# Optimization experiments

Measured on AMD Instinct MI355X. Metric: run time of the kernel, lower is better.

Reference implementation:

```python
import jax, jax.numpy as jnp
import numpy as np
import math

N_HEADS = 8
INPUT_DIM = 128
EMBED_DIM = 128
KEY_DIM = EMBED_DIM // N_HEADS  # 16, val_dim == key_dim
BATCH = 4
GRAPH = 2048


def setup_inputs() -> dict:
    key = jax.random.key(0)
    k1, k2, k3, k4, k5 = jax.random.split(key, 5)
    h = jax.random.normal(k1, (BATCH, GRAPH, INPUT_DIM), dtype=jnp.float32)
    # torch.rand -> uniform [0,1)
    W_query = jax.random.uniform(k2, (N_HEADS, INPUT_DIM, KEY_DIM), dtype=jnp.float32)
    W_key = jax.random.uniform(k3, (N_HEADS, INPUT_DIM, KEY_DIM), dtype=jnp.float32)
    W_val = jax.random.uniform(k4, (N_HEADS, INPUT_DIM, KEY_DIM), dtype=jnp.float32)
    W_out = jax.random.uniform(k5, (N_HEADS, KEY_DIM, EMBED_DIM), dtype=jnp.float32)
    return {"h": h, "W_query": W_query, "W_key": W_key, "W_val": W_val, "W_out": W_out}


def reference(h, W_query, W_key, W_val, W_out):
    # q defaults to h (self-attention)
    norm = 1.0 / math.sqrt(KEY_DIM)
    # per-head projections: [H, B, N, dk]
    Q = jnp.einsum('bnd,hdk->hbnk', h, W_query)
    K = jnp.einsum('bnd,hdk->hbnk', h, W_key)
    V = jnp.einsum('bnd,hdv->hbnv', h, W_val)
    compat = norm * jnp.einsum('hbqk,hbnk->hbqn', Q, K)  # [H, B, Nq, N]
    attn = jax.nn.softmax(compat, axis=-1)
    heads = jnp.einsum('hbqn,hbnv->hbqv', attn, V)  # [H, B, Nq, dv]
    out = jnp.einsum('hbqv,hve->bqe', heads, W_out)  # [B, Nq, E]
    return out
```

## Files before the change

### kernel.cpp

```cpp
#include <hip/hip_runtime.h>

typedef __attribute__((ext_vector_type(4))) float f32x4;
typedef __attribute__((ext_vector_type(8))) short bf16x8;

constexpr int NH = 8, D = 128, DK = 16, B = 4, N = 2048;
constexpr int KTILE = 128;
constexpr int NTILES = N / KTILE;
constexpr int TILE_SHORTS = 6144;
constexpr float QSCALE = 0.36067376022224085f;

__device__ __forceinline__ unsigned short f2bf(float f) {
    union { float f; unsigned u; } v; v.f = f;
    return (unsigned short)((v.u + 0x7fffu + ((v.u >> 16) & 1u)) >> 16);
}
__device__ __forceinline__ float bf2f(unsigned short h) {
    union { unsigned u; float f; } v; v.u = ((unsigned)h) << 16; return v.f;
}
__device__ __forceinline__ unsigned pack2(float a, float b) {
    union { float f; unsigned u; } x, y; x.f = a; y.f = b;
    return (x.u >> 16) | (y.u & 0xFFFF0000u);
}
__device__ __forceinline__ float fexp2(float x) {
    float r; asm("v_exp_f32 %0, %1" : "=v"(r) : "v"(x)); return r;
}

__global__ __launch_bounds__(256) void wprep_kernel(
    const float* __restrict__ Wq, const float* __restrict__ Wk,
    const float* __restrict__ Wv, const float* __restrict__ Wo,
    unsigned short* __restrict__ Wf, unsigned short* __restrict__ Wof)
{
    const int t = blockIdx.x * 256 + threadIdx.x;
    if (t < 49152) {
        const int p = t >> 14, r = t & 16383;
        const int head = r >> 11, d = (r >> 4) & 127, kk = r & 15;
        const float wv = (p == 0 ? Wq : p == 1 ? Wk : Wv)[r];
        const unsigned short hi = f2bf(wv);
        const unsigned short lo = f2bf(wv - bf2f(hi));
        const int c = p * 8 + head, s = d >> 4, dd = d & 15;
        const int ch = dd >> 3, j = dd & 7;
        Wf[((c * 8 + s) * 64 + kk + 16 * ch) * 8 + j] = hi;
        Wf[((c * 8 + s) * 64 + kk + 16 * (2 + ch)) * 8 + j] = lo;
    } else {
        const int r = t - 49152;
        const int head = r >> 11, v = (r >> 7) & 15, e = r & 127;
        const float wv = Wo[r];
        const unsigned short hi = f2bf(wv);
        const unsigned short lo = f2bf(wv - bf2f(hi));
        const int c = e >> 4, s = head, ch = v >> 3, j = v & 7;
        Wof[((c * 8 + s) * 64 + (e & 15) + 16 * ch) * 8 + j] = hi;
        Wof[((c * 8 + s) * 64 + (e & 15) + 16 * (2 + ch)) * 8 + j] = lo;
    }
}

constexpr int GR = 32;
__global__ __launch_bounds__(256) void qkv_gemm(
    const float* __restrict__ h, const unsigned short* __restrict__ Wf,
    float* __restrict__ Q, unsigned short* __restrict__ KV)
{
    const int cg = blockIdx.x % 3;
    const int row0 = (blockIdx.x / 3) * GR;
    const int b = row0 >> 11, n0 = row0 & (N - 1);
    const int t = threadIdx.x, w = t >> 6, l = t & 63;
    __shared__ unsigned short hf[8][2][64][8];

    #pragma unroll
    for (int pass = 0; pass < 4; ++pass) {
        const int rb = pass * 8 + (t >> 5);
        const int d0 = (t & 31) * 4;
        float4 hv = *(const float4*)&h[(size_t)(row0 + rb) * D + d0];
        #pragma unroll
        for (int i = 0; i < 4; ++i) {
            const int d = d0 + i;
            const float x = ((const float*)&hv)[i];
            const unsigned short hi = f2bf(x);
            const unsigned short lo = f2bf(x - bf2f(hi));
            const int s = d >> 4, dd = d & 15, ch = dd >> 3, j = dd & 7;
            hf[s][rb >> 4][(rb & 15) + 16 * ch][j] = hi;
            hf[s][rb >> 4][(rb & 15) + 16 * (2 + ch)][j] = lo;
        }
    }
    __syncthreads();

    f32x4 acc[4];
    #pragma unroll
    for (int i = 0; i < 4; ++i) acc[i] = (f32x4){0.f, 0.f, 0.f, 0.f};

    const int cbase = cg * 8 + (w >> 1) * 4;
    bf16x8 afc[4], afn[4];
    #pragma unroll
    for (int ct = 0; ct < 4; ++ct)
        afc[ct] = *(const bf16x8*)&Wf[(((cbase + ct) * 8 + 0) * 64 + l) * 8];

    for (int s = 0; s < 8; ++s) {
        if (s + 1 < 8) {
            #pragma unroll
            for (int ct = 0; ct < 4; ++ct)
                afn[ct] = *(const bf16x8*)&Wf[(((cbase + ct) * 8 + (s + 1)) * 64 + l) * 8];
        }
        bf16x8 b1 = *(const bf16x8*)&hf[s][w & 1][l][0];
        bf16x8 b2 = *(const bf16x8*)&hf[s][w & 1][l ^ 32][0];
        #pragma unroll
        for (int ct = 0; ct < 4; ++ct) {
            acc[ct] = __builtin_amdgcn_mfma_f32_16x16x32_bf16(afc[ct], b1, acc[ct], 0, 0, 0);
            acc[ct] = __builtin_amdgcn_mfma_f32_16x16x32_bf16(afc[ct], b2, acc[ct], 0, 0, 0);
        }
        #pragma unroll
        for (int ct = 0; ct < 4; ++ct) afc[ct] = afn[ct];
    }

    const int n = n0 + (w & 1) * 16 + (l & 15);
    const int rl = n & 127;
    const int kk0 = (l >> 4) * 4;
    #pragma unroll
    for (int ct = 0; ct < 4; ++ct) {
        const int head = (w >> 1) * 4 + ct;
        const int hb = head * B + b;
        if (cg == 0) {
            float4 o;
            o.x = acc[ct][0]; o.y = acc[ct][1]; o.z = acc[ct][2]; o.w = acc[ct][3];
            *(float4*)&Q[((size_t)hb * N + n) * DK + kk0] = o;
        } else {
            unsigned short* tb = KV + (size_t)hb * NTILES * TILE_SHORTS
                               + (size_t)(n >> 7) * TILE_SHORTS;
            if (cg == 1) {
                const int gs = kk0 >> 3, j0 = kk0 & 7;
                const int kb2 = rl >> 5, kap = rl & 31;
                const int sub = 2 * kb2 + ((kap >> 2) & 1);
                const int row16 = 4 * (kap >> 3) + (kap & 3);
                ushort4 sh, sl;
                unsigned short* shp = (unsigned short*)&sh;
                unsigned short* slp = (unsigned short*)&sl;
                #pragma unroll
                for (int r = 0; r < 4; ++r) {
                    const unsigned short hi = f2bf(acc[ct][r]);
                    shp[r] = hi;
                    slp[r] = f2bf(acc[ct][r] - bf2f(hi));
                }
                *(ushort4*)&tb[sub * 512 + (row16 + 16 * gs) * 8 + j0] = sh;
                *(ushort4*)&tb[sub * 512 + (row16 + 16 * (2 + gs)) * 8 + j0] = sl;
            } else {
                #pragma unroll
                for (int r = 0; r < 4; ++r) {
                    const int kk = kk0 + r;
                    tb[4096 + kk * 128 + ((rl >> 3) ^ (kk & 7)) * 8 + (rl & 7)]
                        = f2bf(acc[ct][r]);
                }
            }
        }
    }
}

__global__ __launch_bounds__(256, 4) void attn_kernel(
    const float* __restrict__ Q, const unsigned short* __restrict__ KV,
    float* __restrict__ Hd)
{
    const int bid = blockIdx.x;
    const int hb = (bid & 7) * 4 + ((bid >> 3) >> 5);
    const int qt = (bid >> 3) & 31;
    const int t = threadIdx.x, w = t >> 6, l = t & 63;
    const int q16 = l & 15, g = l >> 4;
    const size_t qbase = (size_t)hb * N * DK;
    const char* kvb = (const char*)(KV + (size_t)hb * NTILES * TILE_SHORTS);

    __shared__ unsigned short smem[2][TILE_SHORTS];

    const int qrow = qt * 64 + w * 16 + q16;
    bf16x8 qhi, qlo;
    {
        const float* qp = Q + qbase + (size_t)qrow * DK + (g & 1) * 8;
        float4 qa = *(const float4*)qp, qb = *(const float4*)(qp + 4);
        #pragma unroll
        for (int i = 0; i < 8; ++i) {
            const float x = (i < 4 ? ((const float*)&qa)[i] : ((const float*)&qb)[i - 4]) * QSCALE;
            const unsigned short hi = f2bf(x);
            qhi[i] = (short)hi;
            qlo[i] = (short)f2bf(x - bf2f(hi));
        }
    }
    const bf16x8 qf1 = (g < 2) ? qhi : qlo;
    const bf16x8 qf2 = (g < 2) ? qlo : qhi;

    union { unsigned u[4]; bf16x8 v; } ones;
    #pragma unroll
    for (int i = 0; i < 4; ++i) ones.u[i] = 0x3F803F80u;

    f32x4 oacc = {0.f, 0.f, 0.f, 0.f};
    f32x4 lacc = {0.f, 0.f, 0.f, 0.f};
    float m = 0.0f;

    uint4 s0 = *(const uint4*)(kvb + t * 16);
    uint4 s1 = *(const uint4*)(kvb + 4096 + t * 16);
    uint4 s2 = *(const uint4*)(kvb + 8192 + t * 16);
    *(uint4*)((char*)&smem[0][0] + t * 16) = s0;
    *(uint4*)((char*)&smem[0][0] + 4096 + t * 16) = s1;
    *(uint4*)((char*)&smem[0][0] + 8192 + t * 16) = s2;

    int cur = 0;
    for (int tile = 0; tile < NTILES; ++tile) {
        __syncthreads();
        if (tile + 1 < NTILES) {
            const char* gt = kvb + (size_t)(tile + 1) * 12288;
            s0 = *(const uint4*)(gt + t * 16);
            s1 = *(const uint4*)(gt + 4096 + t * 16);
            s2 = *(const uint4*)(gt + 8192 + t * 16);
        }
        const char* buf = (const char*)&smem[cur][0];

        f32x4 aA[4], aB[4];
        const f32x4 minit = {-m, -m, -m, -m};
        __builtin_amdgcn_s_setprio(1);
        #pragma unroll
        for (int kb = 0; kb < 4; ++kb) {
            bf16x8 kA = *(const bf16x8*)(buf + (2 * kb) * 1024 + l * 16);
            bf16x8 kB = *(const bf16x8*)(buf + (2 * kb + 1) * 1024 + l * 16);
            aA[kb] = __builtin_amdgcn_mfma_f32_16x16x32_bf16(kA, qf1, minit, 0, 0, 0);
            aA[kb] = __builtin_amdgcn_mfma_f32_16x16x32_bf16(kA, qf2, aA[kb], 0, 0, 0);
            aB[kb] = __builtin_amdgcn_mfma_f32_16x16x32_bf16(kB, qf1, minit, 0, 0, 0);
            aB[kb] = __builtin_amdgcn_mfma_f32_16x16x32_bf16(kB, qf2, aB[kb], 0, 0, 0);
        }
        __builtin_amdgcn_s_setprio(0);

        float tm = -3.0e38f;
        #pragma unroll
        for (int kb = 0; kb < 4; ++kb) {
            tm = fmaxf(tm, fmaxf(fmaxf(aA[kb][0], aA[kb][1]), fmaxf(aA[kb][2], aA[kb][3])));
            tm = fmaxf(tm, fmaxf(fmaxf(aB[kb][0], aB[kb][1]), fmaxf(aB[kb][2], aB[kb][3])));
        }
        if (tile == 0) {
            float d = fmaxf(tm, __shfl_xor(tm, 16));
            d = fmaxf(d, __shfl_xor(d, 32));
            m = d;
            #pragma unroll
            for (int kb = 0; kb < 4; ++kb) {
                #pragma unroll
                for (int i = 0; i < 4; ++i) { aA[kb][i] -= d; aB[kb][i] -= d; }
            }
        } else if (!__all(tm <= 8.0f)) {
            float d = fmaxf(tm, __shfl_xor(tm, 16));
            d = fmaxf(d, __shfl_xor(d, 32));
            const float dd = fmaxf(d, 0.f);
            const float sc = fexp2(-dd);
            m += dd;
            oacc *= sc;
            lacc *= sc;
            #pragma unroll
            for (int kb = 0; kb < 4; ++kb) {
                #pragma unroll
                for (int i = 0; i < 4; ++i) { aA[kb][i] -= dd; aB[kb][i] -= dd; }
            }
        }
        #pragma unroll
        for (int kb = 0; kb < 4; ++kb) {
            #pragma unroll
            for (int i = 0; i < 4; ++i) {
                aA[kb][i] = fexp2(aA[kb][i]);
                aB[kb][i] = fexp2(aB[kb][i]);
            }
        }
        __builtin_amdgcn_s_setprio(1);
        #pragma unroll
        for (int kb = 0; kb < 4; ++kb) {
            union { unsigned u[4]; bf16x8 v; } pf;
            pf.u[0] = pack2(aA[kb][0], aA[kb][1]);
            pf.u[1] = pack2(aA[kb][2], aA[kb][3]);
            pf.u[2] = pack2(aB[kb][0], aB[kb][1]);
            pf.u[3] = pack2(aB[kb][2], aB[kb][3]);
            bf16x8 vf = *(const bf16x8*)(buf + 8192 + q16 * 256 + (((kb * 4 + g) ^ (q16 & 7)) * 16));
            oacc = __builtin_amdgcn_mfma_f32_16x16x32_bf16(vf, pf.v, oacc, 0, 0, 0);
            lacc = __builtin_amdgcn_mfma_f32_16x16x32_bf16(ones.v, pf.v, lacc, 0, 0, 0);
        }
        __builtin_amdgcn_s_setprio(0);

        if (tile + 1 < NTILES) {
            char* nb = (char*)&smem[cur ^ 1][0];
            *(uint4*)(nb + t * 16) = s0;
            *(uint4*)(nb + 4096 + t * 16) = s1;
            *(uint4*)(nb + 8192 + t * 16) = s2;
        }
        cur ^= 1;
    }

    const float invl = 1.f / lacc[0];
    float4 o;
    o.x = oacc[0] * invl; o.y = oacc[1] * invl;
    o.z = oacc[2] * invl; o.w = oacc[3] * invl;
    *(float4*)(Hd + qbase + (size_t)qrow * DK + g * 4) = o;
}

constexpr int OGR = 16;
__global__ __launch_bounds__(256) void out_gemm(
    const float* __restrict__ Hd, const unsigned short* __restrict__ Wof,
    float* __restrict__ out)
{
    const int row0 = blockIdx.x * OGR;
    const int b = row0 >> 11, n0 = row0 & (N - 1);
    const int t = threadIdx.x, w = t >> 6, l = t & 63;
    __shared__ unsigned short hf[8][64][8];

    #pragma unroll
    for (int pass = 0; pass < 2; ++pass) {
        const int rb = pass * 8 + (t >> 5);
        const int d0 = (t & 31) * 4;
        float4 hv = *(const float4*)&Hd[((size_t)((d0 >> 4) * B + b) * N + (n0 + rb)) * DK + (d0 & 15)];
        #pragma unroll
        for (int i = 0; i < 4; ++i) {
            const int d = d0 + i;
            const float x = ((const float*)&hv)[i];
            const unsigned short hi = f2bf(x);
            const unsigned short lo = f2bf(x - bf2f(hi));
            const int s = d >> 4, dd = d & 15, ch = dd >> 3, j = dd & 7;
            hf[s][rb + 16 * ch][j] = hi;
            hf[s][rb + 16 * (2 + ch)][j] = lo;
        }
    }
    __syncthreads();

    f32x4 acc[2];
    #pragma unroll
    for (int i = 0; i < 2; ++i) acc[i] = (f32x4){0.f, 0.f, 0.f, 0.f};

    bf16x8 afc[2], afn[2];
    #pragma unroll
    for (int ct = 0; ct < 2; ++ct)
        afc[ct] = *(const bf16x8*)&Wof[(((w * 2 + ct) * 8 + 0) * 64 + l) * 8];

    for (int s = 0; s < 8; ++s) {
        if (s + 1 < 8) {
            #pragma unroll
            for (int ct = 0; ct < 2; ++ct)
                afn[ct] = *(const bf16x8*)&Wof[(((w * 2 + ct) * 8 + (s + 1)) * 64 + l) * 8];
        }
        bf16x8 b1 = *(const bf16x8*)&hf[s][l][0];
        bf16x8 b2 = *(const bf16x8*)&hf[s][l ^ 32][0];
        #pragma unroll
        for (int ct = 0; ct < 2; ++ct) {
            acc[ct] = __builtin_amdgcn_mfma_f32_16x16x32_bf16(afc[ct], b1, acc[ct], 0, 0, 0);
            acc[ct] = __builtin_amdgcn_mfma_f32_16x16x32_bf16(afc[ct], b2, acc[ct], 0, 0, 0);
        }
        #pragma unroll
        for (int ct = 0; ct < 2; ++ct) afc[ct] = afn[ct];
    }

    const int n = row0 + (l & 15);
    #pragma unroll
    for (int ct = 0; ct < 2; ++ct) {
        const int c = w * 2 + ct;
        float4 o;
        o.x = acc[ct][0]; o.y = acc[ct][1]; o.z = acc[ct][2]; o.w = acc[ct][3];
        *(float4*)&out[(size_t)n * D + c * 16 + (l >> 4) * 4] = o;
    }
}

extern "C" void kernel_launch(void* const* d_in, const int* in_sizes, int n_in,
                              void* d_out, int out_size, void* d_ws, size_t ws_size,
                              hipStream_t stream) {
    const float* h  = (const float*)d_in[0];
    const float* Wq = (const float*)d_in[1];
    const float* Wk = (const float*)d_in[2];
    const float* Wv = (const float*)d_in[3];
    const float* Wo = (const float*)d_in[4];
    float* out = (float*)d_out;

    char* ws = (char*)d_ws;
    float* Q = (float*)ws;
    unsigned short* KV  = (unsigned short*)(ws + (size_t)4 * 1024 * 1024);
    unsigned short* Wf  = (unsigned short*)(ws + (size_t)10 * 1024 * 1024);
    unsigned short* Wof = (unsigned short*)(ws + (size_t)10 * 1024 * 1024 + 196608);

    wprep_kernel<<<256, 256, 0, stream>>>(Wq, Wk, Wv, Wo, Wf, Wof);
    qkv_gemm<<<(B * N / GR) * 3, 256, 0, stream>>>(h, Wf, Q, KV);
    attn_kernel<<<NH * B * 32, 256, 0, stream>>>(Q, KV, Q);
    out_gemm<<<B * N / OGR, 256, 0, stream>>>(Q, Wof, out);
}
```

Before: 58.21 us.

## Process two query subtiles per attention block to reuse K/V tiles

Each attention block now handles 128 query rows (two 64-row subtiles) instead of 64, so every K/V tile loaded into LDS and every K/V fragment read from shared memory serves twice as many queries. The grid is halved to 512 blocks and the launch bound drops to 2 blocks per SM to allow for the doubled register state. The aim is to cut global and LDS traffic for K/V. The cost is fewer blocks and lower occupancy, which may reduce latency hiding on a GPU with many CUs.

```diff
diff --git a/kernel.cpp b/kernel.cpp
--- a/kernel.cpp
+++ b/kernel.cpp
@@ -150,13 +150,14 @@
     }
 }
 
-__global__ __launch_bounds__(256, 4) void attn_kernel(
+__global__ __launch_bounds__(256, 2) void attn_kernel(
     const float* __restrict__ Q, const unsigned short* __restrict__ KV,
     float* __restrict__ Hd)
 {
     const int bid = blockIdx.x;
-    const int hb = (bid & 7) * 4 + ((bid >> 3) >> 5);
-    const int qt = (bid >> 3) & 31;
+    const int inner = bid >> 3;
+    const int hb = (bid & 7) * 4 + (inner >> 4);
+    const int qt = inner & 15;
     const int t = threadIdx.x, w = t >> 6, l = t & 63;
     const int q16 = l & 15, g = l >> 4;
     const size_t qbase = (size_t)hb * N * DK;
@@ -164,11 +165,13 @@
 
     __shared__ unsigned short smem[2][TILE_SHORTS];
 
-    const int qrow = qt * 64 + w * 16 + q16;
-    bf16x8 qhi, qlo;
-    {
+    bf16x8 qf1[2], qf2[2];
+    #pragma unroll
+    for (int st = 0; st < 2; ++st) {
+        const int qrow = qt * 128 + st * 64 + w * 16 + q16;
         const float* qp = Q + qbase + (size_t)qrow * DK + (g & 1) * 8;
         float4 qa = *(const float4*)qp, qb = *(const float4*)(qp + 4);
+        bf16x8 qhi, qlo;
         #pragma unroll
         for (int i = 0; i < 8; ++i) {
             const float x = (i < 4 ? ((const float*)&qa)[i] : ((const float*)&qb)[i - 4]) * QSCALE;
@@ -176,17 +179,22 @@
             qhi[i] = (short)hi;
             qlo[i] = (short)f2bf(x - bf2f(hi));
         }
-    }
-    const bf16x8 qf1 = (g < 2) ? qhi : qlo;
-    const bf16x8 qf2 = (g < 2) ? qlo : qhi;
+        qf1[st] = (g < 2) ? qhi : qlo;
+        qf2[st] = (g < 2) ? qlo : qhi;
+    }
 
     union { unsigned u[4]; bf16x8 v; } ones;
     #pragma unroll
     for (int i = 0; i < 4; ++i) ones.u[i] = 0x3F803F80u;
 
-    f32x4 oacc = {0.f, 0.f, 0.f, 0.f};
-    f32x4 lacc = {0.f, 0.f, 0.f, 0.f};
-    float m = 0.0f;
+    f32x4 oacc[2], lacc[2];
+    float m[2];
+    #pragma unroll
+    for (int st = 0; st < 2; ++st) {
+        oacc[st] = (f32x4){0.f, 0.f, 0.f, 0.f};
+        lacc[st] = (f32x4){0.f, 0.f, 0.f, 0.f};
+        m[st] = 0.0f;
+    }
 
     uint4 s0 = *(const uint4*)(kvb + t * 16);
     uint4 s1 = *(const uint4*)(kvb + 4096 + t * 16);
@@ -206,70 +214,78 @@
         }
         const char* buf = (const char*)&smem[cur][0];
 
-        f32x4 aA[4], aB[4];
-        const f32x4 minit = {-m, -m, -m, -m};
-        __builtin_amdgcn_s_setprio(1);
+        bf16x8 kA[4], kB[4], vf[4];
         #pragma unroll
         for (int kb = 0; kb < 4; ++kb) {
-            bf16x8 kA = *(const bf16x8*)(buf + (2 * kb) * 1024 + l * 16);
-            bf16x8 kB = *(const bf16x8*)(buf + (2 * kb + 1) * 1024 + l * 16);
-            aA[kb] = __builtin_amdgcn_mfma_f32_16x16x32_bf16(kA, qf1, minit, 0, 0, 0);
-            aA[kb] = __builtin_amdgcn_mfma_f32_16x16x32_bf16(kA, qf2, aA[kb], 0, 0, 0);
-            aB[kb] = __builtin_amdgcn_mfma_f32_16x16x32_bf16(kB, qf1, minit, 0, 0, 0);
-            aB[kb] = __builtin_amdgcn_mfma_f32_16x16x32_bf16(kB, qf2, aB[kb], 0, 0, 0);
-        }
-        __builtin_amdgcn_s_setprio(0);
-
-        float tm = -3.0e38f;
-        #pragma unroll
-        for (int kb = 0; kb < 4; ++kb) {
-            tm = fmaxf(tm, fmaxf(fmaxf(aA[kb][0], aA[kb][1]), fmaxf(aA[kb][2], aA[kb][3])));
-            tm = fmaxf(tm, fmaxf(fmaxf(aB[kb][0], aB[kb][1]), fmaxf(aB[kb][2], aB[kb][3])));
-        }
-        if (tile == 0) {
-            float d = fmaxf(tm, __shfl_xor(tm, 16));
-            d = fmaxf(d, __shfl_xor(d, 32));
-            m = d;
+            kA[kb] = *(const bf16x8*)(buf + (2 * kb) * 1024 + l * 16);
+            kB[kb] = *(const bf16x8*)(buf + (2 * kb + 1) * 1024 + l * 16);
+            vf[kb] = *(const bf16x8*)(buf + 8192 + q16 * 256 + (((kb * 4 + g) ^ (q16 & 7)) * 16));
+        }
+
+        #pragma unroll
+        for (int st = 0; st < 2; ++st) {
+            f32x4 aA[4], aB[4];
+            const f32x4 minit = {-m[st], -m[st], -m[st], -m[st]};
+            __builtin_amdgcn_s_setprio(1);
             #pragma unroll
             for (int kb = 0; kb < 4; ++kb) {
-                #pragma unroll
-                for (int i = 0; i < 4; ++i) { aA[kb][i] -= d; aB[kb][i] -= d; }
-            }
-        } else if (!__all(tm <= 8.0f)) {
-            float d = fmaxf(tm, __shfl_xor(tm, 16));
-            d = fmaxf(d, __shfl_xor(d, 32));
-            const float dd = fmaxf(d, 0.f);
-            const float sc = fexp2(-dd);
-            m += dd;
-            oacc *= sc;
-            lacc *= sc;
+                aA[kb] = __builtin_amdgcn_mfma_f32_16x16x32_bf16(kA[kb], qf1[st], minit, 0, 0, 0);
+                aA[kb] = __builtin_amdgcn_mfma_f32_16x16x32_bf16(kA[kb], qf2[st], aA[kb], 0, 0, 0);
+                aB[kb] = __builtin_amdgcn_mfma_f32_16x16x32_bf16(kB[kb], qf1[st], minit, 0, 0, 0);
+                aB[kb] = __builtin_amdgcn_mfma_f32_16x16x32_bf16(kB[kb], qf2[st], aB[kb], 0, 0, 0);
+            }
+            __builtin_amdgcn_s_setprio(0);
+
+            float tm = -3.0e38f;
             #pragma unroll
             for (int kb = 0; kb < 4; ++kb) {
-                #pragma unroll
-                for (int i = 0; i < 4; ++i) { aA[kb][i] -= dd; aB[kb][i] -= dd; }
-            }
-        }
-        #pragma unroll
-        for (int kb = 0; kb < 4; ++kb) {
-            #pragma unroll
-            for (int i = 0; i < 4; ++i) {
-                aA[kb][i] = fexp2(aA[kb][i]);
-                aB[kb][i] = fexp2(aB[kb][i]);
-            }
-        }
-        __builtin_amdgcn_s_setprio(1);
-        #pragma unroll
-        for (int kb = 0; kb < 4; ++kb) {
-            union { unsigned u[4]; bf16x8 v; } pf;
-            pf.u[0] = pack2(aA[kb][0], aA[kb][1]);
-            pf.u[1] = pack2(aA[kb][2], aA[kb][3]);
-            pf.u[2] = pack2(aB[kb][0], aB[kb][1]);
-            pf.u[3] = pack2(aB[kb][2], aB[kb][3]);
-            bf16x8 vf = *(const bf16x8*)(buf + 8192 + q16 * 256 + (((kb * 4 + g) ^ (q16 & 7)) * 16));
-            oacc = __builtin_amdgcn_mfma_f32_16x16x32_bf16(vf, pf.v, oacc, 0, 0, 0);
-            lacc = __builtin_amdgcn_mfma_f32_16x16x32_bf16(ones.v, pf.v, lacc, 0, 0, 0);
-        }
-        __builtin_amdgcn_s_setprio(0);
+                tm = fmaxf(tm, fmaxf(fmaxf(aA[kb][0], aA[kb][1]), fmaxf(aA[kb][2], aA[kb][3])));
+                tm = fmaxf(tm, fmaxf(fmaxf(aB[kb][0], aB[kb][1]), fmaxf(aB[kb][2], aB[kb][3])));
+            }
+            if (tile == 0) {
+                float d = fmaxf(tm, __shfl_xor(tm, 16));
+                d = fmaxf(d, __shfl_xor(d, 32));
+                m[st] = d;
+                #pragma unroll
+                for (int kb = 0; kb < 4; ++kb) {
+                    #pragma unroll
+                    for (int i = 0; i < 4; ++i) { aA[kb][i] -= d; aB[kb][i] -= d; }
+                }
+            } else if (!__all(tm <= 8.0f)) {
+                float d = fmaxf(tm, __shfl_xor(tm, 16));
+                d = fmaxf(d, __shfl_xor(d, 32));
+                const float dd = fmaxf(d, 0.f);
+                const float sc = fexp2(-dd);
+                m[st] += dd;
+                oacc[st] *= sc;
+                lacc[st] *= sc;
+                #pragma unroll
+                for (int kb = 0; kb < 4; ++kb) {
+                    #pragma unroll
+                    for (int i = 0; i < 4; ++i) { aA[kb][i] -= dd; aB[kb][i] -= dd; }
+                }
+            }
+            #pragma unroll
+            for (int kb = 0; kb < 4; ++kb) {
+                #pragma unroll
+                for (int i = 0; i < 4; ++i) {
+                    aA[kb][i] = fexp2(aA[kb][i]);
+                    aB[kb][i] = fexp2(aB[kb][i]);
+                }
+            }
+            __builtin_amdgcn_s_setprio(1);
+            #pragma unroll
+            for (int kb = 0; kb < 4; ++kb) {
+                union { unsigned u[4]; bf16x8 v; } pf;
+                pf.u[0] = pack2(aA[kb][0], aA[kb][1]);
+                pf.u[1] = pack2(aA[kb][2], aA[kb][3]);
+                pf.u[2] = pack2(aB[kb][0], aB[kb][1]);
+                pf.u[3] = pack2(aB[kb][2], aB[kb][3]);
+                oacc[st] = __builtin_amdgcn_mfma_f32_16x16x32_bf16(vf[kb], pf.v, oacc[st], 0, 0, 0);
+                lacc[st] = __builtin_amdgcn_mfma_f32_16x16x32_bf16(ones.v, pf.v, lacc[st], 0, 0, 0);
+            }
+            __builtin_amdgcn_s_setprio(0);
+        }
 
         if (tile + 1 < NTILES) {
             char* nb = (char*)&smem[cur ^ 1][0];
@@ -280,11 +296,15 @@
         cur ^= 1;
     }
 
-    const float invl = 1.f / lacc[0];
-    float4 o;
-    o.x = oacc[0] * invl; o.y = oacc[1] * invl;
-    o.z = oacc[2] * invl; o.w = oacc[3] * invl;
-    *(float4*)(Hd + qbase + (size_t)qrow * DK + g * 4) = o;
+    #pragma unroll
+    for (int st = 0; st < 2; ++st) {
+        const int qrow = qt * 128 + st * 64 + w * 16 + q16;
+        const float invl = 1.f / lacc[st][0];
+        float4 o;
+        o.x = oacc[st][0] * invl; o.y = oacc[st][1] * invl;
+        o.z = oacc[st][2] * invl; o.w = oacc[st][3] * invl;
+        *(float4*)(Hd + qbase + (size_t)qrow * DK + g * 4) = o;
+    }
 }
 
 constexpr int OGR = 16;
@@ -369,6 +389,6 @@
 
     wprep_kernel<<<256, 256, 0, stream>>>(Wq, Wk, Wv, Wo, Wf, Wof);
     qkv_gemm<<<(B * N / GR) * 3, 256, 0, stream>>>(h, Wf, Q, KV);
-    attn_kernel<<<NH * B * 32, 256, 0, stream>>>(Q, KV, Q);
+    attn_kernel<<<NH * B * 16, 256, 0, stream>>>(Q, KV, Q);
     out_gemm<<<B * N / OGR, 256, 0, stream>>>(Q, Wof, out);
 }
```

Result: slower. 60.77 us (+4.4%).

## Load K/V fragments directly from global memory, dropping LDS double buffer

Applied to the files above, without the earlier changes.

The attention kernel no longer stages each K/V tile through a shared-memory double buffer guarded by block barriers. Each wave now loads its K and V MFMA fragments straight from global memory (relying on L1/L2 caching, since all four waves read the same tile), which removes the __syncthreads, the LDS writes and the LDS reads. In exchange, global traffic to the cache rises about fourfold and there is no explicit prefetch of the next tile, so load latency may be exposed unless the compiler or occupancy hides it.

```diff
diff --git a/kernel.cpp b/kernel.cpp
--- a/kernel.cpp
+++ b/kernel.cpp
@@ -162,8 +162,6 @@
     const size_t qbase = (size_t)hb * N * DK;
     const char* kvb = (const char*)(KV + (size_t)hb * NTILES * TILE_SHORTS);
 
-    __shared__ unsigned short smem[2][TILE_SHORTS];
-
     const int qrow = qt * 64 + w * 16 + q16;
     bf16x8 qhi, qlo;
     {
@@ -188,35 +186,27 @@
     f32x4 lacc = {0.f, 0.f, 0.f, 0.f};
     float m = 0.0f;
 
-    uint4 s0 = *(const uint4*)(kvb + t * 16);
-    uint4 s1 = *(const uint4*)(kvb + 4096 + t * 16);
-    uint4 s2 = *(const uint4*)(kvb + 8192 + t * 16);
-    *(uint4*)((char*)&smem[0][0] + t * 16) = s0;
-    *(uint4*)((char*)&smem[0][0] + 4096 + t * 16) = s1;
-    *(uint4*)((char*)&smem[0][0] + 8192 + t * 16) = s2;
-
-    int cur = 0;
+    const int vsw = 8192 + q16 * 256;
+
     for (int tile = 0; tile < NTILES; ++tile) {
-        __syncthreads();
-        if (tile + 1 < NTILES) {
-            const char* gt = kvb + (size_t)(tile + 1) * 12288;
-            s0 = *(const uint4*)(gt + t * 16);
-            s1 = *(const uint4*)(gt + 4096 + t * 16);
-            s2 = *(const uint4*)(gt + 8192 + t * 16);
-        }
-        const char* buf = (const char*)&smem[cur][0];
+        const char* tb = kvb + (size_t)tile * 12288;
+        bf16x8 kA[4], kB[4], vf[4];
+        #pragma unroll
+        for (int kb = 0; kb < 4; ++kb) {
+            kA[kb] = *(const bf16x8*)(tb + (2 * kb) * 1024 + l * 16);
+            kB[kb] = *(const bf16x8*)(tb + (2 * kb + 1) * 1024 + l * 16);
+            vf[kb] = *(const bf16x8*)(tb + vsw + (((kb * 4 + g) ^ (q16 & 7)) * 16));
+        }
 
         f32x4 aA[4], aB[4];
         const f32x4 minit = {-m, -m, -m, -m};
         __builtin_amdgcn_s_setprio(1);
         #pragma unroll
         for (int kb = 0; kb < 4; ++kb) {
-            bf16x8 kA = *(const bf16x8*)(buf + (2 * kb) * 1024 + l * 16);
-            bf16x8 kB = *(const bf16x8*)(buf + (2 * kb + 1) * 1024 + l * 16);
-            aA[kb] = __builtin_amdgcn_mfma_f32_16x16x32_bf16(kA, qf1, minit, 0, 0, 0);
-            aA[kb] = __builtin_amdgcn_mfma_f32_16x16x32_bf16(kA, qf2, aA[kb], 0, 0, 0);
-            aB[kb] = __builtin_amdgcn_mfma_f32_16x16x32_bf16(kB, qf1, minit, 0, 0, 0);
-            aB[kb] = __builtin_amdgcn_mfma_f32_16x16x32_bf16(kB, qf2, aB[kb], 0, 0, 0);
+            aA[kb] = __builtin_amdgcn_mfma_f32_16x16x32_bf16(kA[kb], qf1, minit, 0, 0, 0);
+            aA[kb] = __builtin_amdgcn_mfma_f32_16x16x32_bf16(kA[kb], qf2, aA[kb], 0, 0, 0);
+            aB[kb] = __builtin_amdgcn_mfma_f32_16x16x32_bf16(kB[kb], qf1, minit, 0, 0, 0);
+            aB[kb] = __builtin_amdgcn_mfma_f32_16x16x32_bf16(kB[kb], qf2, aB[kb], 0, 0, 0);
         }
         __builtin_amdgcn_s_setprio(0);
 
@@ -265,19 +255,10 @@
             pf.u[1] = pack2(aA[kb][2], aA[kb][3]);
             pf.u[2] = pack2(aB[kb][0], aB[kb][1]);
             pf.u[3] = pack2(aB[kb][2], aB[kb][3]);
-            bf16x8 vf = *(const bf16x8*)(buf + 8192 + q16 * 256 + (((kb * 4 + g) ^ (q16 & 7)) * 16));
-            oacc = __builtin_amdgcn_mfma_f32_16x16x32_bf16(vf, pf.v, oacc, 0, 0, 0);
+            oacc = __builtin_amdgcn_mfma_f32_16x16x32_bf16(vf[kb], pf.v, oacc, 0, 0, 0);
             lacc = __builtin_amdgcn_mfma_f32_16x16x32_bf16(ones.v, pf.v, lacc, 0, 0, 0);
         }
         __builtin_amdgcn_s_setprio(0);
-
-        if (tile + 1 < NTILES) {
-            char* nb = (char*)&smem[cur ^ 1][0];
-            *(uint4*)(nb + t * 16) = s0;
-            *(uint4*)(nb + 4096 + t * 16) = s1;
-            *(uint4*)(nb + 8192 + t * 16) = s2;
-        }
-        cur ^= 1;
     }
 
     const float invl = 1.f / lacc[0];
```

Measured after the change: 60.30 us. 1.04x slower.
